# Kernel tuning notes

Hardware: AMD Instinct MI355X
Metric: run time of the kernel (lower is better)

## Reference

```python
import jax, jax.numpy as jnp
import numpy as np

NHEADS = 8
MIN_DEPTH = 0.5
MAX_DEPTH = 100.0


def _gather(img, xi, yi, nb, W, H):
    valid = (xi >= 0) & (xi < W) & (yi >= 0) & (yi < H)
    xc = jnp.clip(xi, 0, W - 1)
    yc = jnp.clip(yi, 0, H - 1)
    vals = img[nb, :, yc, xc]  # (N,Ho,Wo,C) - advanced idx dims come first
    return vals * valid[..., None].astype(img.dtype)


def grid_sample(img, grid, mode='bilinear'):
    # img: (N,C,H,W), grid: (N,Ho,Wo,2) in [-1,1], zeros padding, align_corners=True
    N, C, H, W = img.shape
    gx = (grid[..., 0] + 1.0) * 0.5 * (W - 1)
    gy = (grid[..., 1] + 1.0) * 0.5 * (H - 1)
    nb = jnp.arange(N)[:, None, None]
    if mode == 'nearest':
        out = _gather(img, jnp.round(gx).astype(jnp.int32), jnp.round(gy).astype(jnp.int32), nb, W, H)
    else:
        x0 = jnp.floor(gx); y0 = jnp.floor(gy)
        wx = (gx - x0)[..., None]; wy = (gy - y0)[..., None]
        x0i = x0.astype(jnp.int32); y0i = y0.astype(jnp.int32)
        g00 = _gather(img, x0i, y0i, nb, W, H)
        g01 = _gather(img, x0i + 1, y0i, nb, W, H)
        g10 = _gather(img, x0i, y0i + 1, nb, W, H)
        g11 = _gather(img, x0i + 1, y0i + 1, nb, W, H)
        out = (1 - wy) * ((1 - wx) * g00 + wx * g01) + wy * ((1 - wx) * g10 + wx * g11)
    return jnp.transpose(out, (0, 3, 1, 2))  # (N,C,Ho,Wo)


def _avg3(x):
    # 3x3 avg pool, stride 1, reflect pad 1 (output same HxW)
    xp = jnp.pad(x, ((0, 0), (0, 0), (1, 1), (1, 1)), mode='reflect')
    return jax.lax.reduce_window(xp, 0.0, jax.lax.add, (1, 1, 3, 3), (1, 1, 1, 1), 'VALID') / 9.0


def ssim_loss(x, y, C1=1e-4, C2=9e-4):
    mx, my = _avg3(x), _avg3(y)
    sx = _avg3(x * x) - mx * mx
    sy = _avg3(y * y) - my * my
    sxy = _avg3(x * y) - mx * my
    num = (2 * mx * my + C1) * (2 * sxy + C2)
    den = (mx * mx + my * my + C1) * (sx + sy + C2)
    return jnp.clip((1.0 - num / den) * 0.5, 0.0, 1.0)


def prepare_b(x):
    d, c, h, w = x.shape
    return x.transpose(0, 2, 3, 1).reshape(d, h * w, c)  # (seq=d, batch=h*w, c)


def layer_norm(x, g, b, eps=1e-5):
    m = x.mean(-1, keepdims=True)
    v = ((x - m) ** 2).mean(-1, keepdims=True)
    return (x - m) * jax.lax.rsqrt(v + eps) * g + b


def attention(q_in, kv_in, w_qkv, b_qkv, w_o, b_o):
    # q_in: (Lq,B,C), kv_in: (Lk,B,C)
    C = q_in.shape[-1]
    hd = C // NHEADS
    q = q_in @ w_qkv[:C].T + b_qkv[:C]
    kv = kv_in @ w_qkv[C:].T + b_qkv[C:]
    k, v = jnp.split(kv, 2, axis=-1)
    Lq, B = q.shape[0], q.shape[1]
    Lk = k.shape[0]
    q = (q * (hd ** -0.5)).reshape(Lq, B, NHEADS, hd)
    k = k.reshape(Lk, B, NHEADS, hd)
    v = v.reshape(Lk, B, NHEADS, hd)
    attn = jnp.einsum('wnhc,vnhc->nhwv', q, k)  # (B,H,Lq,Lk)
    p = jax.nn.softmax(attn, axis=-1)
    out = jnp.einsum('nhwv,vnhc->wnhc', p, v).reshape(Lq, B, C)
    out = out @ w_o.T + b_o
    raw = attn.sum(axis=1)  # (B,Lq,Lk)
    return out, raw


def _forward(feat1, feat2, coords, sa_in_w, sa_in_b, sa_out_w, sa_out_b, sa_ln_g, sa_ln_b,
             ca_in_w, ca_in_b, ca_out_w, ca_out_b, ca_ln_g, ca_ln_b, num_bins):
    bs, C, h, w = feat1.shape
    cg = jnp.where(coords < -1.0, -2.0, coords)
    cg = jnp.where(cg > 1.0, 2.0, cg)
    rep_feat2 = jnp.broadcast_to(feat2, (num_bins, C, h, w))
    warped = grid_sample(rep_feat2, cg, 'bilinear')  # (num_bins,C,h,w)
    ones = jnp.ones((num_bins, 1, h, w), feat1.dtype)
    warped_mask = grid_sample(ones, cg, 'nearest')
    # SSIM cost volume (no-grad side outputs)
    x = jnp.broadcast_to(feat1, warped.shape)
    ssim_volume = jax.lax.stop_gradient(ssim_loss(x, warped).mean(axis=1)[None])  # (1,num_bins,h,w)
    idx = jnp.argmin(ssim_volume, axis=1)  # (1,h,w)
    depth = jnp.exp(np.float32(np.log(MIN_DEPTH)) + np.float32(np.log(MAX_DEPTH / MIN_DEPTH)) * idx.astype(feat1.dtype) / (num_bins - 1))
    lowest_cost = 1.0 / depth
    f1 = prepare_b(feat1)   # (bs, h*w, C)
    f2 = prepare_b(warped)  # (num_bins, h*w, C)
    raw = None
    L = sa_in_w.shape[0]
    for i in range(L):
        f1n = layer_norm(f1, sa_ln_g[i], sa_ln_b[i])
        o, _ = attention(f1n, f1n, sa_in_w[i], sa_in_b[i], sa_out_w[i], sa_out_b[i])
        f1 = f1 + o
        f1n = layer_norm(f1, ca_ln_g[i], ca_ln_b[i])
        f2n = layer_norm(f2, ca_ln_g[i], ca_ln_b[i])
        o, raw = attention(f1n, f2n, ca_in_w[i], ca_in_b[i], ca_out_w[i], ca_out_b[i])
        f1 = f1 + o
    attn_weight = raw.reshape(bs, h, w, num_bins)
    return attn_weight, warped_mask, lowest_cost, ssim_volume


def setup_inputs():
    key = jax.random.key(0)
    ks = jax.random.split(key, 16)
    C, L, NB, H, W = 128, 6, 64, 48, 160
    s = 0.02
    return {
        'feat1': jax.random.normal(ks[0], (1, C, H, W), jnp.float32),
        'feat2': jax.random.normal(ks[1], (1, C, H, W), jnp.float32),
        'coords': jax.random.uniform(ks[2], (NB, H, W, 2), jnp.float32) * 2.4 - 1.2,
        'sa_in_w': jax.random.normal(ks[3], (L, 3 * C, C), jnp.float32) * s,
        'sa_in_b': jax.random.normal(ks[4], (L, 3 * C), jnp.float32) * s,
        'sa_out_w': jax.random.normal(ks[5], (L, C, C), jnp.float32) * s,
        'sa_out_b': jax.random.normal(ks[6], (L, C), jnp.float32) * s,
        'sa_ln_g': jnp.ones((L, C), jnp.float32),
        'sa_ln_b': jnp.zeros((L, C), jnp.float32),
        'ca_in_w': jax.random.normal(ks[7], (L, 3 * C, C), jnp.float32) * s,
        'ca_in_b': jax.random.normal(ks[8], (L, 3 * C), jnp.float32) * s,
        'ca_out_w': jax.random.normal(ks[9], (L, C, C), jnp.float32) * s,
        'ca_out_b': jax.random.normal(ks[10], (L, C), jnp.float32) * s,
        'ca_ln_g': jnp.ones((L, C), jnp.float32),
        'ca_ln_b': jnp.zeros((L, C), jnp.float32),
        'num_bins': NB,
    }


def reference(feat1, feat2, coords, sa_in_w, sa_in_b, sa_out_w, sa_out_b, sa_ln_g, sa_ln_b,
              ca_in_w, ca_in_b, ca_out_w, ca_out_b, ca_ln_g, ca_ln_b, num_bins):
    return _forward(feat1, feat2, coords, sa_in_w, sa_in_b, sa_out_w, sa_out_b, sa_ln_g, sa_ln_b,
                    ca_in_w, ca_in_b, ca_out_w, ca_out_b, ca_ln_g, ca_ln_b, num_bins)
```

## Files before the change

kernel.cpp:

```cpp
#include <hip/hip_runtime.h>

constexpr int kH  = 48;
constexpr int kW  = 160;
constexpr int kP  = 7680;
constexpr int kC  = 128;
constexpr int kNB = 64;
constexpr int kNH = 8;
constexpr int kNL = 6;

constexpr long long OFF_F1T = 0;
constexpr long long OFF_F2T = 983040;
constexpr long long OFF_F2  = 1966080;
constexpr long long OFF_MU  = OFF_F2 + 62914560LL;
constexpr long long OFF_SIG = OFF_MU + 491520LL;
constexpr long long OFF_WTS = OFF_SIG + 491520LL;
constexpr int WSA2 = 0;
constexpr int WQ2  = 8192;
constexpr int WKU  = 16384;
constexpr int WV2  = 24576;
constexpr int WO2  = 32768;
constexpr int BSA  = 40960;
constexpr int BQ   = 41088;
constexpr int BK   = 41216;
constexpr int BV   = 41344;
constexpr int WTS_STRIDE = 41472;

constexpr long long OUT_ATT  = 0;
constexpr long long OUT_MASK = 491520;
constexpr long long OUT_LC   = 983040;
constexpr long long OUT_SSIM = 990720;

typedef _Float16 h2v __attribute__((ext_vector_type(2)));
typedef __fp16 p2v __attribute__((ext_vector_type(2)));
typedef float f2v __attribute__((ext_vector_type(2)));
typedef __fp16 h8 __attribute__((ext_vector_type(8)));
typedef float fx16 __attribute__((ext_vector_type(16)));
union U32H2 { unsigned u; h2v h; };
union U32P2 { unsigned u; p2v h; };

__device__ __forceinline__ float fdot2(unsigned a, unsigned b, float c) {
  U32H2 ua; ua.u = a; U32H2 ub; ub.u = b;
  return __builtin_amdgcn_fdot2(ua.h, ub.h, c, false);
}
__device__ __forceinline__ unsigned pkrtz(float a, float b) {
  U32P2 t; t.h = __builtin_amdgcn_cvt_pkrtz(a, b); return t.u;
}
__device__ __forceinline__ f2v h2f(unsigned u) {
  U32P2 t; t.u = u; f2v r; r.x = (float)t.h.x; r.y = (float)t.h.y; return r;
}
__device__ __forceinline__ unsigned short f2h(float x) {
  U32P2 t; t.h = __builtin_amdgcn_cvt_pkrtz(x, 0.f); return (unsigned short)(t.u & 0xffffu);
}
__device__ __forceinline__ void wb() {
  __asm__ __volatile__("" ::: "memory");
  __builtin_amdgcn_wave_barrier();
  __asm__ __volatile__("" ::: "memory");
}

__global__ __launch_bounds__(256) void k_transpose(const float* __restrict__ feat1,
                                                   const float* __restrict__ feat2,
                                                   float* __restrict__ f1t,
                                                   float* __restrict__ f2t) {
  __shared__ float t1[32][33], t2[32][33];
  const int p0 = blockIdx.x * 32, c0 = blockIdx.y * 32;
  const int r = threadIdx.x >> 5, col = threadIdx.x & 31;
#pragma unroll
  for (int rr = r; rr < 32; rr += 8) {
    t1[rr][col] = feat1[(c0 + rr) * kP + p0 + col];
    t2[rr][col] = feat2[(c0 + rr) * kP + p0 + col];
  }
  __syncthreads();
#pragma unroll
  for (int rr = r; rr < 32; rr += 8) {
    f1t[(p0 + rr) * kC + c0 + col] = t1[col][rr];
    f2t[(p0 + rr) * kC + c0 + col] = t2[col][rr];
  }
}

__device__ __forceinline__ float redsum128(float v, float* red2) {
#pragma unroll
  for (int off = 32; off > 0; off >>= 1) v += __shfl_xor(v, off);
  int t = threadIdx.x;
  if ((t & 63) == 0) red2[t >> 6] = v;
  __syncthreads();
  float r = red2[0] + red2[1];
  __syncthreads();
  return r;
}

__global__ __launch_bounds__(128) void k_fold(
    const float* __restrict__ saw_, const float* __restrict__ sab_,
    const float* __restrict__ sow_, const float* __restrict__ sob_,
    const float* __restrict__ slg_, const float* __restrict__ slb_,
    const float* __restrict__ caw_, const float* __restrict__ cab_,
    const float* __restrict__ clg_, const float* __restrict__ clb_,
    const float* __restrict__ cow_, float* __restrict__ wts) {
  int i = blockIdx.x >> 7, d = blockIdx.x & 127, c = threadIdx.x;
  const float* saw = saw_ + (long long)i * 384 * kC;
  const float* sab = sab_ + i * 384;
  const float* sow = sow_ + i * kC * kC;
  const float* sob = sob_ + i * kC;
  const float* slg = slg_ + i * kC;
  const float* slb = slb_ + i * kC;
  const float* caw = caw_ + (long long)i * 384 * kC;
  const float* cab = cab_ + i * 384;
  const float* clg = clg_ + i * kC;
  const float* clb = clb_ + i * kC;
  const float* cow = cow_ + i * kC * kC;
  float* WL = wts + (long long)i * WTS_STRIDE;
  __shared__ float red2[2];

  int jstd = (c >> 3) * 1024 + d * 8 + (c & 7);

  float acc = 0.f;
  for (int m = 0; m < kC; m++) acc += sow[d * kC + m] * saw[(256 + m) * kC + c];
  float t1 = redsum128(acc * slb[c] + sow[d * kC + c] * sab[256 + c], red2);
  if (c == 0) WL[BSA + d] = t1 + sob[d];
  ((unsigned short*)(WL + WSA2))[jstd] = f2h(acc * slg[c]);

  float wq = caw[d * kC + c];
  float t2 = redsum128(wq * clb[c], red2);
  if (c == 0) WL[BQ + d] = 0.25f * (t2 + cab[d]);
  ((unsigned short*)(WL + WQ2))[jstd] = f2h(0.25f * wq * clg[c]);

  float wk = caw[(kC + d) * kC + c];
  float t3 = redsum128(wk * clb[c], red2);
  if (c == 0) WL[BK + d] = t3 + cab[kC + d];
  {
    int h = d >> 4, o = d & 15;
    ((unsigned short*)(WL + WKU))[h * 2048 + c * 16 + o] = f2h(wk * clg[c]);
  }

  float wv = caw[(2 * kC + d) * kC + c];
  float t4 = redsum128(wv * clb[c], red2);
  if (c == 0) WL[BV + d] = t4 + cab[2 * kC + d];
  ((unsigned short*)(WL + WV2))[jstd] = f2h(wv * clg[c]);

  ((unsigned short*)(WL + WO2))[jstd] = f2h(cow[d * kC + c]);
}

__global__ __launch_bounds__(256) void k_warp(const float* __restrict__ f2t,
                                              const float* __restrict__ coords,
                                              float* __restrict__ F2, float* __restrict__ mu,
                                              float* __restrict__ sig, float* __restrict__ maskout) {
  int wave = threadIdx.x >> 6, lane = threadIdx.x & 63;
  int pix = blockIdx.x * 4 + wave;
  int b = blockIdx.y;
  long long bp = (long long)b * kP + pix;
  float cx = coords[bp * 2], cy = coords[bp * 2 + 1];
  cx = (cx < -1.f) ? -2.f : cx;
  cx = (cx > 1.f) ? 2.f : cx;
  cy = (cy < -1.f) ? -2.f : cy;
  cy = (cy > 1.f) ? 2.f : cy;
  float gx = (cx + 1.f) * 0.5f * (float)(kW - 1);
  float gy = (cy + 1.f) * 0.5f * (float)(kH - 1);
  float x0f = floorf(gx), y0f = floorf(gy);
  float wx = gx - x0f, wy = gy - y0f;
  int x0 = (int)x0f, y0 = (int)y0f;
  int x1 = x0 + 1, y1 = y0 + 1;
  float vx0 = (x0 >= 0 && x0 < kW) ? 1.f : 0.f;
  float vx1 = (x1 >= 0 && x1 < kW) ? 1.f : 0.f;
  float vy0 = (y0 >= 0 && y0 < kH) ? 1.f : 0.f;
  float vy1 = (y1 >= 0 && y1 < kH) ? 1.f : 0.f;
  int x0c = min(max(x0, 0), kW - 1), x1c = min(max(x1, 0), kW - 1);
  int y0c = min(max(y0, 0), kH - 1), y1c = min(max(y1, 0), kH - 1);
  float w00 = (1.f - wy) * (1.f - wx) * vx0 * vy0;
  float w01 = (1.f - wy) * wx * vx1 * vy0;
  float w10 = wy * (1.f - wx) * vx0 * vy1;
  float w11 = wy * wx * vx1 * vy1;
  const float2* r00 = (const float2*)(f2t + (y0c * kW + x0c) * kC);
  const float2* r01 = (const float2*)(f2t + (y0c * kW + x1c) * kC);
  const float2* r10 = (const float2*)(f2t + (y1c * kW + x0c) * kC);
  const float2* r11 = (const float2*)(f2t + (y1c * kW + x1c) * kC);
  float2 g00 = r00[lane], g01 = r01[lane], g10 = r10[lane], g11 = r11[lane];
  float v0 = w00 * g00.x + w01 * g01.x + w10 * g10.x + w11 * g11.x;
  float v1 = w00 * g00.y + w01 * g01.y + w10 * g10.y + w11 * g11.y;
  float s = v0 + v1, s2 = v0 * v0 + v1 * v1;
#pragma unroll
  for (int off = 32; off > 0; off >>= 1) {
    s += __shfl_xor(s, off);
    s2 += __shfl_xor(s2, off);
  }
  float m = s * (1.f / 128.f);
  float var = s2 * (1.f / 128.f) - m * m;
  float rs = rsqrtf(var + 1e-5f);
  float2 o;
  o.x = (v0 - m) * rs;
  o.y = (v1 - m) * rs;
  ((float2*)(F2 + bp * kC))[lane] = o;
  if (lane == 0) {
    mu[bp] = m;
    sig[bp] = sqrtf(var + 1e-5f);
    int xi = (int)rintf(gx), yi = (int)rintf(gy);
    maskout[bp] = (xi >= 0 && xi < kW && yi >= 0 && yi < kH) ? 1.f : 0.f;
  }
}

__global__ __launch_bounds__(256) void k_ssim(const float* __restrict__ f1t,
                                              const float* __restrict__ F2,
                                              const float* __restrict__ mu,
                                              const float* __restrict__ sig,
                                              float* __restrict__ ssimout) {
  const int lane = threadIdx.x & 63;
  const int y = blockIdx.x * 4 + (threadIdx.x >> 6);
  const int b = blockIdx.y;
  const int ym = (y == 0) ? 1 : y - 1;
  const int yp = (y == kH - 1) ? kH - 2 : y + 1;
  const long long bb = (long long)b * kP;
  const float* f1m = f1t + (ym * kW) * kC + 2 * lane;
  const float* f10 = f1t + (y * kW) * kC + 2 * lane;
  const float* f1p = f1t + (yp * kW) * kC + 2 * lane;
  const float* F2m = F2 + (bb + ym * kW) * kC + 2 * lane;
  const float* F20 = F2 + (bb + y * kW) * kC + 2 * lane;
  const float* F2p = F2 + (bb + yp * kW) * kC + 2 * lane;
  const float* mum = mu + bb + ym * kW;
  const float* mu0 = mu + bb + y * kW;
  const float* mup = mu + bb + yp * kW;
  const float* sgm = sig + bb + ym * kW;
  const float* sg0 = sig + bb + y * kW;
  const float* sgp = sig + bb + yp * kW;
  float* outrow = ssimout + bb + y * kW;

  f2v C[3][5];

  auto colsum = [&](int x, f2v* Cc) {
    f2v am = *(const f2v*)(f1m + (size_t)x * kC);
    f2v a0 = *(const f2v*)(f10 + (size_t)x * kC);
    f2v ap = *(const f2v*)(f1p + (size_t)x * kC);
    f2v fm = *(const f2v*)(F2m + (size_t)x * kC);
    f2v f0 = *(const f2v*)(F20 + (size_t)x * kC);
    f2v fp = *(const f2v*)(F2p + (size_t)x * kC);
    f2v wm = fm * sgm[x] + mum[x];
    f2v w0 = f0 * sg0[x] + mu0[x];
    f2v wp = fp * sgp[x] + mup[x];
    Cc[0] = am + a0 + ap;
    Cc[1] = wm + w0 + wp;
    Cc[2] = am * am + a0 * a0 + ap * ap;
    Cc[3] = wm * wm + w0 * w0 + wp * wp;
    Cc[4] = am * wm + a0 * w0 + ap * wp;
  };

  auto emit = [&](int xo, f2v s0, f2v s1, f2v s2, f2v s3, f2v s4) {
    const float inv9 = 1.f / 9.f;
    f2v mx = s0 * inv9, my = s1 * inv9;
    f2v vx = s2 * inv9 - mx * mx;
    f2v vy = s3 * inv9 - my * my;
    f2v vxy = s4 * inv9 - mx * my;
    f2v num = (2.f * mx * my + 1e-4f) * (2.f * vxy + 9e-4f);
    f2v den = (mx * mx + my * my + 1e-4f) * (vx + vy + 9e-4f);
    f2v val = (1.f - num / den) * 0.5f;
    float t = fminf(fmaxf(val.x, 0.f), 1.f) + fminf(fmaxf(val.y, 0.f), 1.f);
#pragma unroll
    for (int o = 32; o > 0; o >>= 1) t += __shfl_xor(t, o);
    if (lane == 0) outrow[xo] = t * (1.f / 128.f);
  };

  colsum(0, C[0]);
  colsum(1, C[1]);
  emit(0, C[0][0] + 2.f * C[1][0], C[0][1] + 2.f * C[1][1], C[0][2] + 2.f * C[1][2],
       C[0][3] + 2.f * C[1][3], C[0][4] + 2.f * C[1][4]);
#pragma unroll 3
  for (int x = 2; x < kW; ++x) {
    colsum(x, C[x % 3]);
    emit(x - 1, C[0][0] + C[1][0] + C[2][0], C[0][1] + C[1][1] + C[2][1],
         C[0][2] + C[1][2] + C[2][2], C[0][3] + C[1][3] + C[2][3],
         C[0][4] + C[1][4] + C[2][4]);
  }
  emit(kW - 1, C[0][0] + 2.f * C[2][0], C[0][1] + 2.f * C[2][1], C[0][2] + 2.f * C[2][2],
       C[0][3] + 2.f * C[2][3], C[0][4] + 2.f * C[2][4]);
}

__global__ __launch_bounds__(256) void k_argmin(const float* __restrict__ ssim,
                                                float* __restrict__ lc) {
  int pix = blockIdx.x * 256 + threadIdx.x;
  float best = ssim[pix];
  int bi = 0;
  for (int b = 1; b < kNB; b++) {
    float v = ssim[b * kP + pix];
    if (v < best) { best = v; bi = b; }
  }
  float depth = expf(-0.69314718f + (5.2983174f * (float)bi) / 63.0f);
  lc[pix] = 1.f / depth;
}


__device__ __forceinline__ f2v gemmW(int l, const unsigned* __restrict__ inb,
                                     const unsigned* __restrict__ W, float b0, float b1) {
  float a0 = b0, a1 = b1, c0 = 0.f, c1 = 0.f;
  const unsigned* wp = W + l * 8;
#pragma unroll
  for (int j = 0; j < 16; j += 2) {
    uint4 inA = *(const uint4*)(inb + 4 * j);
    uint4 inB = *(const uint4*)(inb + 4 * j + 4);
    uint4 wa = *(const uint4*)(wp + j * 512);
    uint4 wc = *(const uint4*)(wp + j * 512 + 4);
    uint4 wa2 = *(const uint4*)(wp + j * 512 + 512);
    uint4 wc2 = *(const uint4*)(wp + j * 512 + 516);
    a0 = fdot2(inA.x, wa.x, a0);  a0 = fdot2(inA.y, wa.y, a0);
    a0 = fdot2(inA.z, wa.z, a0);  a0 = fdot2(inA.w, wa.w, a0);
    a1 = fdot2(inA.x, wc.x, a1);  a1 = fdot2(inA.y, wc.y, a1);
    a1 = fdot2(inA.z, wc.z, a1);  a1 = fdot2(inA.w, wc.w, a1);
    c0 = fdot2(inB.x, wa2.x, c0); c0 = fdot2(inB.y, wa2.y, c0);
    c0 = fdot2(inB.z, wa2.z, c0); c0 = fdot2(inB.w, wa2.w, c0);
    c1 = fdot2(inB.x, wc2.x, c1); c1 = fdot2(inB.y, wc2.y, c1);
    c1 = fdot2(inB.z, wc2.z, c1); c1 = fdot2(inB.w, wc2.w, c1);
  }
  f2v r; r.x = a0 + c0; r.y = a1 + c1; return r;
}

__device__ __forceinline__ void ln_store(int l, f2v X, unsigned* xhq) {
  float s = X.x + X.y, s2 = X.x * X.x + X.y * X.y;
#pragma unroll
  for (int o = 32; o > 0; o >>= 1) { s += __shfl_xor(s, o); s2 += __shfl_xor(s2, o); }
  float m = s * 0.0078125f;
  float var = s2 * 0.0078125f - m * m;
  float rs = rsqrtf(var + 1e-5f);
  xhq[l] = pkrtz((X.x - m) * rs, (X.y - m) * rs);
}

__global__ __launch_bounds__(64) void k_attn(const float* __restrict__ F2g,
                                             const float* __restrict__ f1t,
                                             const float* __restrict__ wts,
                                             const float* __restrict__ cab_out,
                                             float* __restrict__ attn_out) {
  __shared__ __align__(16) unsigned F2s[64 * 64];
  __shared__ __align__(16) unsigned upb[512];
  __shared__ __align__(16) unsigned xhq[64];

  const int l = threadIdx.x;
  const int pix = blockIdx.x;

  {
#pragma unroll 4
    for (int r = 0; r < 64; ++r) {
      float2 v = *(const float2*)(F2g + ((long long)r * kP + pix) * kC + 2 * l);
      F2s[r * 64 + (l ^ (4 * (r & 15)))] = pkrtz(v.x, v.y);
    }
  }
  f2v X;
  { float2 xv = ((const float2*)(f1t + (long long)pix * kC))[l]; X.x = xv.x; X.y = xv.y; }
  wb();

  float chsum = 0.f;
  float* pf = (float*)upb;
  const int mrow = l & 31;
  const int kg = l >> 5;
  const int rbase = 4 * kg;

  for (int ly = 0; ly < kNL; ++ly) {
    const float* WL = wts + (long long)ly * WTS_STRIDE;

    ln_store(l, X, xhq);
    wb();
    {
      float2 bv = ((const float2*)(WL + BSA))[l];
      f2v o = gemmW(l, xhq, (const unsigned*)(WL + WSA2), bv.x, bv.y);
      X += o;
    }
    wb();
    ln_store(l, X, xhq);
    wb();
    f2v q;
    {
      float2 bv = ((const float2*)(WL + BQ))[l];
      q = gemmW(l, xhq, (const unsigned*)(WL + WQ2), bv.x, bv.y);
    }
    if (ly == kNL - 1) {
      float2 bk = ((const float2*)(WL + BK))[l];
      float cp = q.x * bk.x + q.y * bk.y;
#pragma unroll
      for (int o = 32; o > 0; o >>= 1) cp += __shfl_xor(cp, o);
      chsum = cp;
    }
    xhq[l] = pkrtz(q.x, q.y);
    wb();

    {
      const unsigned* KU = (const unsigned*)(WL + WKU);
#pragma unroll
      for (int h = 0; h < kNH; ++h) {
        uint4 q0 = *(const uint4*)(xhq + h * 8);
        uint4 q1 = *(const uint4*)(xhq + h * 8 + 4);
        const unsigned* w0 = KU + (h * 128 + 2 * l) * 8;
        uint4 a0 = ((const uint4*)w0)[0], a1 = ((const uint4*)w0)[1];
        uint4 b0 = ((const uint4*)w0)[2], b1 = ((const uint4*)w0)[3];
        float u0 = 0.f, u1 = 0.f, u2 = 0.f, u3 = 0.f;
        u0 = fdot2(q0.x, a0.x, u0); u0 = fdot2(q0.y, a0.y, u0);
        u0 = fdot2(q0.z, a0.z, u0); u0 = fdot2(q0.w, a0.w, u0);
        u2 = fdot2(q1.x, a1.x, u2); u2 = fdot2(q1.y, a1.y, u2);
        u2 = fdot2(q1.z, a1.z, u2); u2 = fdot2(q1.w, a1.w, u2);
        u1 = fdot2(q0.x, b0.x, u1); u1 = fdot2(q0.y, b0.y, u1);
        u1 = fdot2(q0.z, b0.z, u1); u1 = fdot2(q0.w, b0.w, u1);
        u3 = fdot2(q1.x, b1.x, u3); u3 = fdot2(q1.y, b1.y, u3);
        u3 = fdot2(q1.z, b1.z, u3); u3 = fdot2(q1.w, b1.w, u3);
        upb[h * 64 + (l ^ (4 * h))] = pkrtz(u0 + u2, u1 + u3);
      }
    }
    wb();

    fx16 acc0 = (fx16)0.f, acc1 = (fx16)0.f;
    {
      const int hn = mrow & 7;
      const int sw = 4 * (mrow & 15);
      const int usw = 4 * hn;
#pragma unroll
      for (int kc = 0; kc < 8; ++kc) {
        const int cp = kc * 8 + kg * 4;
        h8 Bv = *(const h8*)(upb + hn * 64 + (cp ^ usw));
        h8 A0 = *(const h8*)(F2s + mrow * 64 + (cp ^ sw));
        h8 A1 = *(const h8*)(F2s + (mrow + 32) * 64 + (cp ^ sw));
        acc0 = __builtin_amdgcn_mfma_f32_32x32x16_f16(A0, Bv, acc0, 0, 0, 0);
        acc1 = __builtin_amdgcn_mfma_f32_32x32x16_f16(A1, Bv, acc1, 0, 0, 0);
      }
    }
    if (ly == kNL - 1) {
      wb();
      if (mrow < 8) {
#pragma unroll
        for (int r = 0; r < 16; ++r) {
          int row = (r & 3) + 8 * (r >> 2) + rbase;
          pf[mrow * 64 + row] = acc0[r];
          pf[mrow * 64 + 32 + row] = acc1[r];
        }
      }
      wb();
      float rsum = chsum;
#pragma unroll
      for (int h = 0; h < kNH; ++h) rsum += pf[h * 64 + l];
      attn_out[(long long)pix * 64 + l] = rsum;
      return;
    }
    {
      float mx = acc0[0];
#pragma unroll
      for (int r = 0; r < 16; ++r) { mx = fmaxf(mx, acc0[r]); mx = fmaxf(mx, acc1[r]); }
      mx = fmaxf(mx, __shfl_xor(mx, 32));
      float pv0[16], pv1[16];
      float sm = 0.f;
#pragma unroll
      for (int r = 0; r < 16; ++r) {
        pv0[r] = __expf(acc0[r] - mx); sm += pv0[r];
        pv1[r] = __expf(acc1[r] - mx); sm += pv1[r];
      }
      sm += __shfl_xor(sm, 32);
      float inv = 1.f / sm;
      wb();
      if (mrow < 8) {
#pragma unroll
        for (int r = 0; r < 16; ++r) {
          int row = (r & 3) + 8 * (r >> 2) + rbase;
          pf[row * 8 + mrow] = pv0[r] * inv;
          pf[(32 + row) * 8 + mrow] = pv1[r] * inv;
        }
      }
    }
    wb();
    {
      const int half = l >> 5, lb = l & 31;
      f2v wA[8], wB[8];
#pragma unroll
      for (int h = 0; h < kNH; ++h) { wA[h] = (f2v)0.f; wB[h] = (f2v)0.f; }
#pragma unroll 2
      for (int t = 0; t < 32; ++t) {
        int b = half * 32 + t;
        uint2 fv = *(const uint2*)(F2s + b * 64 + ((2 * lb) ^ (4 * (b & 15))));
        f2v fA = h2f(fv.x), fB = h2f(fv.y);
        float4 pA = *(const float4*)(pf + b * 8);
        float4 pB = *(const float4*)(pf + b * 8 + 4);
        wA[0] += fA * pA.x; wB[0] += fB * pA.x;
        wA[1] += fA * pA.y; wB[1] += fB * pA.y;
        wA[2] += fA * pA.z; wB[2] += fB * pA.z;
        wA[3] += fA * pA.w; wB[3] += fB * pA.w;
        wA[4] += fA * pB.x; wB[4] += fB * pB.x;
        wA[5] += fA * pB.y; wB[5] += fB * pB.y;
        wA[6] += fA * pB.z; wB[6] += fB * pB.z;
        wA[7] += fA * pB.w; wB[7] += fB * pB.w;
      }
#pragma unroll
      for (int h = 0; h < kNH; ++h) {
        wA[h].x += __shfl_xor(wA[h].x, 32);
        wA[h].y += __shfl_xor(wA[h].y, 32);
        wB[h].x += __shfl_xor(wB[h].x, 32);
        wB[h].y += __shfl_xor(wB[h].y, 32);
      }
      wb();
#pragma unroll
      for (int hh = 0; hh < 4; ++hh) {
        int h = half * 4 + hh;
        uint2 pk;
        pk.x = pkrtz(wA[h].x, wA[h].y);
        pk.y = pkrtz(wB[h].x, wB[h].y);
        *(uint2*)(upb + h * 64 + ((2 * lb) ^ (4 * h))) = pk;
      }
    }
    wb();
    {
      const int h = l >> 3;
      const unsigned* wrow = upb + h * 64;
      const unsigned* WV = (const unsigned*)(WL + WV2) + l * 8;
      float2 bv = ((const float2*)(WL + BV))[l];
      float a0 = bv.x, a1 = bv.y, c0 = 0.f, c1 = 0.f;
      const int sw = 4 * h;
#pragma unroll
      for (int j = 0; j < 16; j += 2) {
        uint4 inA = *(const uint4*)(wrow + ((4 * j) ^ sw));
        uint4 inB = *(const uint4*)(wrow + ((4 * j + 4) ^ sw));
        uint4 wa = *(const uint4*)(WV + j * 512);
        uint4 wc = *(const uint4*)(WV + j * 512 + 4);
        uint4 wa2 = *(const uint4*)(WV + j * 512 + 512);
        uint4 wc2 = *(const uint4*)(WV + j * 512 + 516);
        a0 = fdot2(inA.x, wa.x, a0);  a0 = fdot2(inA.y, wa.y, a0);
        a0 = fdot2(inA.z, wa.z, a0);  a0 = fdot2(inA.w, wa.w, a0);
        a1 = fdot2(inA.x, wc.x, a1);  a1 = fdot2(inA.y, wc.y, a1);
        a1 = fdot2(inA.z, wc.z, a1);  a1 = fdot2(inA.w, wc.w, a1);
        c0 = fdot2(inB.x, wa2.x, c0); c0 = fdot2(inB.y, wa2.y, c0);
        c0 = fdot2(inB.z, wa2.z, c0); c0 = fdot2(inB.w, wa2.w, c0);
        c1 = fdot2(inB.x, wc2.x, c1); c1 = fdot2(inB.y, wc2.y, c1);
        c1 = fdot2(inB.z, wc2.z, c1); c1 = fdot2(inB.w, wc2.w, c1);
      }
      xhq[l] = pkrtz(a0 + c0, a1 + c1);
    }
    wb();
    {
      float2 bv = ((const float2*)(cab_out + ly * kC))[l];
      f2v o = gemmW(l, xhq, (const unsigned*)(WL + WO2), bv.x, bv.y);
      X += o;
    }
    wb();
  }
}

extern "C" void kernel_launch(void* const* d_in, const int* in_sizes, int n_in, void* d_out,
                              int out_size, void* d_ws, size_t ws_size, hipStream_t stream) {
  (void)in_sizes; (void)n_in; (void)out_size; (void)ws_size;
  const float* feat1 = (const float*)d_in[0];
  const float* feat2 = (const float*)d_in[1];
  const float* coords = (const float*)d_in[2];
  const float* sa_in_w = (const float*)d_in[3];
  const float* sa_in_b = (const float*)d_in[4];
  const float* sa_out_w = (const float*)d_in[5];
  const float* sa_out_b = (const float*)d_in[6];
  const float* sa_ln_g = (const float*)d_in[7];
  const float* sa_ln_b = (const float*)d_in[8];
  const float* ca_in_w = (const float*)d_in[9];
  const float* ca_in_b = (const float*)d_in[10];
  const float* ca_out_w = (const float*)d_in[11];
  const float* ca_out_b = (const float*)d_in[12];
  const float* ca_ln_g = (const float*)d_in[13];
  const float* ca_ln_b = (const float*)d_in[14];

  float* out = (float*)d_out;
  float* ws = (float*)d_ws;
  float* f1t = ws + OFF_F1T;
  float* f2t = ws + OFF_F2T;
  float* F2 = ws + OFF_F2;
  float* mu = ws + OFF_MU;
  float* sig = ws + OFF_SIG;
  float* wts = ws + OFF_WTS;

  float* att = out + OUT_ATT;
  float* mask = out + OUT_MASK;
  float* lc = out + OUT_LC;
  float* ssim = out + OUT_SSIM;

  dim3 gt(240, 4);
  k_transpose<<<gt, 256, 0, stream>>>(feat1, feat2, f1t, f2t);
  k_fold<<<kNL * 128, 128, 0, stream>>>(sa_in_w, sa_in_b, sa_out_w, sa_out_b, sa_ln_g, sa_ln_b,
                                        ca_in_w, ca_in_b, ca_ln_g, ca_ln_b, ca_out_w, wts);
  dim3 g1(1920, 64);
  k_warp<<<g1, 256, 0, stream>>>(f2t, coords, F2, mu, sig, mask);
  dim3 g2(12, 64);
  k_ssim<<<g2, 256, 0, stream>>>(f1t, F2, mu, sig, ssim);
  k_argmin<<<30, 256, 0, stream>>>(ssim, lc);
  k_attn<<<kP, 64, 0, stream>>>(F2, f1t, wts, ca_out_b, att);
}
```

Baseline: 899.4 us.

## Stage layer weights into LDS with async double-buffering and reorder F2 pixel-major

The attention kernel now runs four pixels per 256-thread block. Per-layer fp16 weights are streamed in chunks into a double-buffered LDS region with global_load_lds, so the four waves share one copy instead of each reading weights from global memory. The warped feature tensor F2 is now written pixel-major so each pixel's 64 bins are contiguous. The attention kernel reads them directly from global and converts to fp16 on the fly, dropping the per-block LDS copy. The weight packing in the fold kernel is reordered to match the chunked LDS layout. The cost is block-wide __syncthreads between chunks and more global reads of F2 inside the layer loop, while k_ssim now reads F2 with a strided pattern.

```diff
diff --git a/kernel.cpp b/kernel.cpp
--- a/kernel.cpp
+++ b/kernel.cpp
@@ -7,6 +7,7 @@
 constexpr int kNB = 64;
 constexpr int kNH = 8;
 constexpr int kNL = 6;
+constexpr int kFS = kNB * kC;
 
 constexpr long long OFF_F1T = 0;
 constexpr long long OFF_F2T = 983040;
@@ -45,9 +46,6 @@
 __device__ __forceinline__ unsigned pkrtz(float a, float b) {
   U32P2 t; t.h = __builtin_amdgcn_cvt_pkrtz(a, b); return t.u;
 }
-__device__ __forceinline__ f2v h2f(unsigned u) {
-  U32P2 t; t.u = u; f2v r; r.x = (float)t.h.x; r.y = (float)t.h.y; return r;
-}
 __device__ __forceinline__ unsigned short f2h(float x) {
   U32P2 t; t.h = __builtin_amdgcn_cvt_pkrtz(x, 0.f); return (unsigned short)(t.u & 0xffffu);
 }
@@ -55,6 +53,19 @@
   __asm__ __volatile__("" ::: "memory");
   __builtin_amdgcn_wave_barrier();
   __asm__ __volatile__("" ::: "memory");
+}
+
+typedef __attribute__((address_space(1))) const void gvoid_t;
+typedef __attribute__((address_space(3))) void svoid_t;
+__device__ __forceinline__ void gl_lds16(const unsigned* g, unsigned* s) {
+  __builtin_amdgcn_global_load_lds((gvoid_t*)g, (svoid_t*)s, 16, 0, 0);
+}
+__device__ __forceinline__ void stage_chunk(const unsigned* W32, int c, unsigned* buf,
+                                            int w, int l) {
+  const unsigned* s = W32 + c * 2048 + w * 512 + l * 4;
+  unsigned* d = buf + w * 512;
+  gl_lds16(s, d);
+  gl_lds16(s + 256, d + 256);
 }
 
 __global__ __launch_bounds__(256) void k_transpose(const float* __restrict__ feat1,
@@ -110,7 +121,7 @@
   float* WL = wts + (long long)i * WTS_STRIDE;
   __shared__ float red2[2];
 
-  int jstd = (c >> 3) * 1024 + d * 8 + (c & 7);
+  int jstd = (c >> 3) * 1024 + (d & 1) * 512 + (d >> 1) * 8 + (c & 7);
 
   float acc = 0.f;
   for (int m = 0; m < kC; m++) acc += sow[d * kC + m] * saw[(256 + m) * kC + c];
@@ -127,8 +138,10 @@
   float t3 = redsum128(wk * clb[c], red2);
   if (c == 0) WL[BK + d] = t3 + cab[kC + d];
   {
-    int h = d >> 4, o = d & 15;
-    ((unsigned short*)(WL + WKU))[h * 2048 + c * 16 + o] = f2h(wk * clg[c]);
+    int h = d >> 4, o = d & 15, op = o >> 1;
+    int q = (c & 1) * 2 + (op >> 2);
+    ((unsigned short*)(WL + WKU))[h * 2048 + q * 512 + (c >> 1) * 8 + (op & 3) * 2 + (o & 1)] =
+        f2h(wk * clg[c]);
   }
 
   float wv = caw[(2 * kC + d) * kC + c];
@@ -141,7 +154,8 @@
 
 __global__ __launch_bounds__(256) void k_warp(const float* __restrict__ f2t,
                                               const float* __restrict__ coords,
-                                              float* __restrict__ F2, float* __restrict__ mu,
+                                              float* __restrict__ F2,
+                                              float* __restrict__ mu,
                                               float* __restrict__ sig, float* __restrict__ maskout) {
   int wave = threadIdx.x >> 6, lane = threadIdx.x & 63;
   int pix = blockIdx.x * 4 + wave;
@@ -187,7 +201,7 @@
   float2 o;
   o.x = (v0 - m) * rs;
   o.y = (v1 - m) * rs;
-  ((float2*)(F2 + bp * kC))[lane] = o;
+  ((float2*)(F2 + ((long long)pix * kNB + b) * kC))[lane] = o;
   if (lane == 0) {
     mu[bp] = m;
     sig[bp] = sqrtf(var + 1e-5f);
@@ -210,9 +224,9 @@
   const float* f1m = f1t + (ym * kW) * kC + 2 * lane;
   const float* f10 = f1t + (y * kW) * kC + 2 * lane;
   const float* f1p = f1t + (yp * kW) * kC + 2 * lane;
-  const float* F2m = F2 + (bb + ym * kW) * kC + 2 * lane;
-  const float* F20 = F2 + (bb + y * kW) * kC + 2 * lane;
-  const float* F2p = F2 + (bb + yp * kW) * kC + 2 * lane;
+  const float* F2m = F2 + ((long long)(ym * kW) * kNB + b) * kC + 2 * lane;
+  const float* F20 = F2 + ((long long)(y * kW) * kNB + b) * kC + 2 * lane;
+  const float* F2p_ = F2 + ((long long)(yp * kW) * kNB + b) * kC + 2 * lane;
   const float* mum = mu + bb + ym * kW;
   const float* mu0 = mu + bb + y * kW;
   const float* mup = mu + bb + yp * kW;
@@ -227,9 +241,9 @@
     f2v am = *(const f2v*)(f1m + (size_t)x * kC);
     f2v a0 = *(const f2v*)(f10 + (size_t)x * kC);
     f2v ap = *(const f2v*)(f1p + (size_t)x * kC);
-    f2v fm = *(const f2v*)(F2m + (size_t)x * kC);
-    f2v f0 = *(const f2v*)(F20 + (size_t)x * kC);
-    f2v fp = *(const f2v*)(F2p + (size_t)x * kC);
+    f2v fm = *(const f2v*)(F2m + (size_t)x * kFS);
+    f2v f0 = *(const f2v*)(F20 + (size_t)x * kFS);
+    f2v fp = *(const f2v*)(F2p_ + (size_t)x * kFS);
     f2v wm = fm * sgm[x] + mum[x];
     f2v w0 = f0 * sg0[x] + mu0[x];
     f2v wp = fp * sgp[x] + mup[x];
@@ -284,29 +298,7 @@
 }
 
 
-__device__ __forceinline__ f2v gemmW(int l, const unsigned* __restrict__ inb,
-                                     const unsigned* __restrict__ W, float b0, float b1) {
-  float a0 = b0, a1 = b1, c0 = 0.f, c1 = 0.f;
-  const unsigned* wp = W + l * 8;
-#pragma unroll
-  for (int j = 0; j < 16; j += 2) {
-    uint4 inA = *(const uint4*)(inb + 4 * j);
-    uint4 inB = *(const uint4*)(inb + 4 * j + 4);
-    uint4 wa = *(const uint4*)(wp + j * 512);
-    uint4 wc = *(const uint4*)(wp + j * 512 + 4);
-    uint4 wa2 = *(const uint4*)(wp + j * 512 + 512);
-    uint4 wc2 = *(const uint4*)(wp + j * 512 + 516);
-    a0 = fdot2(inA.x, wa.x, a0);  a0 = fdot2(inA.y, wa.y, a0);
-    a0 = fdot2(inA.z, wa.z, a0);  a0 = fdot2(inA.w, wa.w, a0);
-    a1 = fdot2(inA.x, wc.x, a1);  a1 = fdot2(inA.y, wc.y, a1);
-    a1 = fdot2(inA.z, wc.z, a1);  a1 = fdot2(inA.w, wc.w, a1);
-    c0 = fdot2(inB.x, wa2.x, c0); c0 = fdot2(inB.y, wa2.y, c0);
-    c0 = fdot2(inB.z, wa2.z, c0); c0 = fdot2(inB.w, wa2.w, c0);
-    c1 = fdot2(inB.x, wc2.x, c1); c1 = fdot2(inB.y, wc2.y, c1);
-    c1 = fdot2(inB.z, wc2.z, c1); c1 = fdot2(inB.w, wc2.w, c1);
-  }
-  f2v r; r.x = a0 + c0; r.y = a1 + c1; return r;
-}
+constexpr int NW = 4;
 
 __device__ __forceinline__ void ln_store(int l, f2v X, unsigned* xhq) {
   float s = X.x + X.y, s2 = X.x * X.x + X.y * X.y;
@@ -318,54 +310,94 @@
   xhq[l] = pkrtz((X.x - m) * rs, (X.y - m) * rs);
 }
 
-__global__ __launch_bounds__(64) void k_attn(const float* __restrict__ F2g,
-                                             const float* __restrict__ f1t,
-                                             const float* __restrict__ wts,
-                                             const float* __restrict__ cab_out,
-                                             float* __restrict__ attn_out) {
-  __shared__ __align__(16) unsigned F2s[64 * 64];
-  __shared__ __align__(16) unsigned upb[512];
-  __shared__ __align__(16) unsigned xhq[64];
-
-  const int l = threadIdx.x;
-  const int pix = blockIdx.x;
-
-  {
-#pragma unroll 4
-    for (int r = 0; r < 64; ++r) {
-      float2 v = *(const float2*)(F2g + ((long long)r * kP + pix) * kC + 2 * l);
-      F2s[r * 64 + (l ^ (4 * (r & 15)))] = pkrtz(v.x, v.y);
-    }
-  }
-  f2v X;
-  { float2 xv = ((const float2*)(f1t + (long long)pix * kC))[l]; X.x = xv.x; X.y = xv.y; }
-  wb();
-
-  float chsum = 0.f;
+__device__ __forceinline__ void dot16(uint4 inA, uint4 inB, uint4 wa, uint4 wc,
+                                      uint4 wa2, uint4 wc2,
+                                      float& a0, float& a1, float& c0, float& c1) {
+  a0 = fdot2(inA.x, wa.x, a0);  a0 = fdot2(inA.y, wa.y, a0);
+  a0 = fdot2(inA.z, wa.z, a0);  a0 = fdot2(inA.w, wa.w, a0);
+  a1 = fdot2(inA.x, wc.x, a1);  a1 = fdot2(inA.y, wc.y, a1);
+  a1 = fdot2(inA.z, wc.z, a1);  a1 = fdot2(inA.w, wc.w, a1);
+  c0 = fdot2(inB.x, wa2.x, c0); c0 = fdot2(inB.y, wa2.y, c0);
+  c0 = fdot2(inB.z, wa2.z, c0); c0 = fdot2(inB.w, wa2.w, c0);
+  c1 = fdot2(inB.x, wc2.x, c1); c1 = fdot2(inB.y, wc2.y, c1);
+  c1 = fdot2(inB.z, wc2.z, c1); c1 = fdot2(inB.w, wc2.w, c1);
+}
+
+__device__ __forceinline__ void gemm_chunk(const unsigned* inb, const unsigned* wbp, int l,
+                                           float& a0, float& a1, float& c0, float& c1) {
+#pragma unroll
+  for (int jj = 0; jj < 4; jj += 2) {
+    uint4 inA = *(const uint4*)(inb + 4 * jj);
+    uint4 inB = *(const uint4*)(inb + 4 * jj + 4);
+    const unsigned* w0 = wbp + jj * 512 + l * 4;
+    uint4 wa = *(const uint4*)(w0);
+    uint4 wc = *(const uint4*)(w0 + 256);
+    uint4 wa2 = *(const uint4*)(w0 + 512);
+    uint4 wc2 = *(const uint4*)(w0 + 768);
+    dot16(inA, inB, wa, wc, wa2, wc2, a0, a1, c0, c1);
+  }
+}
+
+__global__ __launch_bounds__(256, 4) void k_attn(const float* __restrict__ F2f,
+                                                 const float* __restrict__ f1t,
+                                                 const float* __restrict__ wts,
+                                                 const float* __restrict__ cab_out,
+                                                 float* __restrict__ attn_out) {
+  __shared__ __align__(16) unsigned shw[NW * 576];
+  __shared__ __align__(16) unsigned wbuf[2][2048];
+
+  const int tid = threadIdx.x;
+  const int w = tid >> 6, l = tid & 63;
+  const int pix = blockIdx.x * NW + w;
+  unsigned* upb = shw + w * 576;
+  unsigned* xhq = upb + 512;
   float* pf = (float*)upb;
+  const float* F2p = F2f + (long long)pix * kFS;
+
   const int mrow = l & 31;
   const int kg = l >> 5;
   const int rbase = 4 * kg;
 
+  f2v X;
+  { float2 xv = ((const float2*)(f1t + (long long)pix * kC))[l]; X.x = xv.x; X.y = xv.y; }
+
+  stage_chunk((const unsigned*)wts, 0, wbuf[0], w, l);
+  __syncthreads();
+
+  float chsum = 0.f;
   for (int ly = 0; ly < kNL; ++ly) {
     const float* WL = wts + (long long)ly * WTS_STRIDE;
+    const unsigned* W32 = (const unsigned*)WL;
+    const bool last = (ly == kNL - 1);
 
     ln_store(l, X, xhq);
     wb();
     {
       float2 bv = ((const float2*)(WL + BSA))[l];
-      f2v o = gemmW(l, xhq, (const unsigned*)(WL + WSA2), bv.x, bv.y);
-      X += o;
-    }
-    wb();
+      float a0 = bv.x, a1 = bv.y, c0 = 0.f, c1 = 0.f;
+#pragma unroll
+      for (int c = 0; c < 4; ++c) {
+        stage_chunk(W32, c + 1, wbuf[(c + 1) & 1], w, l);
+        gemm_chunk(xhq + 16 * c, wbuf[c & 1], l, a0, a1, c0, c1);
+        __syncthreads();
+      }
+      X.x += a0 + c0; X.y += a1 + c1;
+    }
     ln_store(l, X, xhq);
     wb();
     f2v q;
     {
       float2 bv = ((const float2*)(WL + BQ))[l];
-      q = gemmW(l, xhq, (const unsigned*)(WL + WQ2), bv.x, bv.y);
-    }
-    if (ly == kNL - 1) {
+      float a0 = bv.x, a1 = bv.y, c0 = 0.f, c1 = 0.f;
+#pragma unroll
+      for (int c = 4; c < 8; ++c) {
+        stage_chunk(W32, c + 1, wbuf[(c + 1) & 1], w, l);
+        gemm_chunk(xhq + 16 * (c - 4), wbuf[c & 1], l, a0, a1, c0, c1);
+        __syncthreads();
+      }
+      q.x = a0 + c0; q.y = a1 + c1;
+    }
+    if (last) {
       float2 bk = ((const float2*)(WL + BK))[l];
       float cp = q.x * bk.x + q.y * bk.y;
 #pragma unroll
@@ -375,45 +407,58 @@
     xhq[l] = pkrtz(q.x, q.y);
     wb();
 
-    {
-      const unsigned* KU = (const unsigned*)(WL + WKU);
-#pragma unroll
-      for (int h = 0; h < kNH; ++h) {
+#pragma unroll
+    for (int c = 8; c < 12; ++c) {
+      if (!(last && c == 11)) stage_chunk(W32, c + 1, wbuf[(c + 1) & 1], w, l);
+      const unsigned* wbp = wbuf[c & 1];
+#pragma unroll
+      for (int hh = 0; hh < 2; ++hh) {
+        const int h = (c - 8) * 2 + hh;
         uint4 q0 = *(const uint4*)(xhq + h * 8);
         uint4 q1 = *(const uint4*)(xhq + h * 8 + 4);
-        const unsigned* w0 = KU + (h * 128 + 2 * l) * 8;
-        uint4 a0 = ((const uint4*)w0)[0], a1 = ((const uint4*)w0)[1];
-        uint4 b0 = ((const uint4*)w0)[2], b1 = ((const uint4*)w0)[3];
+        const unsigned* w0 = wbp + hh * 1024 + l * 4;
+        uint4 av0 = *(const uint4*)(w0);
+        uint4 av1 = *(const uint4*)(w0 + 256);
+        uint4 bv0 = *(const uint4*)(w0 + 512);
+        uint4 bv1 = *(const uint4*)(w0 + 768);
         float u0 = 0.f, u1 = 0.f, u2 = 0.f, u3 = 0.f;
-        u0 = fdot2(q0.x, a0.x, u0); u0 = fdot2(q0.y, a0.y, u0);
-        u0 = fdot2(q0.z, a0.z, u0); u0 = fdot2(q0.w, a0.w, u0);
-        u2 = fdot2(q1.x, a1.x, u2); u2 = fdot2(q1.y, a1.y, u2);
-        u2 = fdot2(q1.z, a1.z, u2); u2 = fdot2(q1.w, a1.w, u2);
-        u1 = fdot2(q0.x, b0.x, u1); u1 = fdot2(q0.y, b0.y, u1);
-        u1 = fdot2(q0.z, b0.z, u1); u1 = fdot2(q0.w, b0.w, u1);
-        u3 = fdot2(q1.x, b1.x, u3); u3 = fdot2(q1.y, b1.y, u3);
-        u3 = fdot2(q1.z, b1.z, u3); u3 = fdot2(q1.w, b1.w, u3);
+        u0 = fdot2(q0.x, av0.x, u0); u0 = fdot2(q0.y, av0.y, u0);
+        u0 = fdot2(q0.z, av0.z, u0); u0 = fdot2(q0.w, av0.w, u0);
+        u2 = fdot2(q1.x, av1.x, u2); u2 = fdot2(q1.y, av1.y, u2);
+        u2 = fdot2(q1.z, av1.z, u2); u2 = fdot2(q1.w, av1.w, u2);
+        u1 = fdot2(q0.x, bv0.x, u1); u1 = fdot2(q0.y, bv0.y, u1);
+        u1 = fdot2(q0.z, bv0.z, u1); u1 = fdot2(q0.w, bv0.w, u1);
+        u3 = fdot2(q1.x, bv1.x, u3); u3 = fdot2(q1.y, bv1.y, u3);
+        u3 = fdot2(q1.z, bv1.z, u3); u3 = fdot2(q1.w, bv1.w, u3);
         upb[h * 64 + (l ^ (4 * h))] = pkrtz(u0 + u2, u1 + u3);
       }
-    }
-    wb();
+      __syncthreads();
+    }
 
     fx16 acc0 = (fx16)0.f, acc1 = (fx16)0.f;
     {
       const int hn = mrow & 7;
-      const int sw = 4 * (mrow & 15);
       const int usw = 4 * hn;
+      const float* pA0 = F2p + mrow * kC + kg * 8;
+      const float* pA1 = F2p + (mrow + 32) * kC + kg * 8;
 #pragma unroll
       for (int kc = 0; kc < 8; ++kc) {
         const int cp = kc * 8 + kg * 4;
         h8 Bv = *(const h8*)(upb + hn * 64 + (cp ^ usw));
-        h8 A0 = *(const h8*)(F2s + mrow * 64 + (cp ^ sw));
-        h8 A1 = *(const h8*)(F2s + (mrow + 32) * 64 + (cp ^ sw));
-        acc0 = __builtin_amdgcn_mfma_f32_32x32x16_f16(A0, Bv, acc0, 0, 0, 0);
-        acc1 = __builtin_amdgcn_mfma_f32_32x32x16_f16(A1, Bv, acc1, 0, 0, 0);
-      }
-    }
-    if (ly == kNL - 1) {
+        float4 fa = *(const float4*)(pA0 + kc * 16);
+        float4 fb = *(const float4*)(pA0 + kc * 16 + 4);
+        float4 fc = *(const float4*)(pA1 + kc * 16);
+        float4 fd = *(const float4*)(pA1 + kc * 16 + 4);
+        union { unsigned u[4]; h8 h; } A0u, A1u;
+        A0u.u[0] = pkrtz(fa.x, fa.y); A0u.u[1] = pkrtz(fa.z, fa.w);
+        A0u.u[2] = pkrtz(fb.x, fb.y); A0u.u[3] = pkrtz(fb.z, fb.w);
+        A1u.u[0] = pkrtz(fc.x, fc.y); A1u.u[1] = pkrtz(fc.z, fc.w);
+        A1u.u[2] = pkrtz(fd.x, fd.y); A1u.u[3] = pkrtz(fd.z, fd.w);
+        acc0 = __builtin_amdgcn_mfma_f32_32x32x16_f16(A0u.h, Bv, acc0, 0, 0, 0);
+        acc1 = __builtin_amdgcn_mfma_f32_32x32x16_f16(A1u.h, Bv, acc1, 0, 0, 0);
+      }
+    }
+    if (last) {
       wb();
       if (mrow < 8) {
 #pragma unroll
@@ -457,14 +502,16 @@
     wb();
     {
       const int half = l >> 5, lb = l & 31;
+      const float* F2c = F2p + 4 * lb;
       f2v wA[8], wB[8];
 #pragma unroll
       for (int h = 0; h < kNH; ++h) { wA[h] = (f2v)0.f; wB[h] = (f2v)0.f; }
 #pragma unroll 2
       for (int t = 0; t < 32; ++t) {
         int b = half * 32 + t;
-        uint2 fv = *(const uint2*)(F2s + b * 64 + ((2 * lb) ^ (4 * (b & 15))));
-        f2v fA = h2f(fv.x), fB = h2f(fv.y);
+        float4 fv = *(const float4*)(F2c + b * kC);
+        f2v fA, fB;
+        fA.x = fv.x; fA.y = fv.y; fB.x = fv.z; fB.y = fv.w;
         float4 pA = *(const float4*)(pf + b * 8);
         float4 pB = *(const float4*)(pf + b * 8 + 4);
         wA[0] += fA * pA.x; wB[0] += fB * pA.x;
@@ -495,38 +542,42 @@
     }
     wb();
     {
-      const int h = l >> 3;
+      const int h = l >> 3, sw = 4 * h;
       const unsigned* wrow = upb + h * 64;
-      const unsigned* WV = (const unsigned*)(WL + WV2) + l * 8;
       float2 bv = ((const float2*)(WL + BV))[l];
       float a0 = bv.x, a1 = bv.y, c0 = 0.f, c1 = 0.f;
-      const int sw = 4 * h;
-#pragma unroll
-      for (int j = 0; j < 16; j += 2) {
-        uint4 inA = *(const uint4*)(wrow + ((4 * j) ^ sw));
-        uint4 inB = *(const uint4*)(wrow + ((4 * j + 4) ^ sw));
-        uint4 wa = *(const uint4*)(WV + j * 512);
-        uint4 wc = *(const uint4*)(WV + j * 512 + 4);
-        uint4 wa2 = *(const uint4*)(WV + j * 512 + 512);
-        uint4 wc2 = *(const uint4*)(WV + j * 512 + 516);
-        a0 = fdot2(inA.x, wa.x, a0);  a0 = fdot2(inA.y, wa.y, a0);
-        a0 = fdot2(inA.z, wa.z, a0);  a0 = fdot2(inA.w, wa.w, a0);
-        a1 = fdot2(inA.x, wc.x, a1);  a1 = fdot2(inA.y, wc.y, a1);
-        a1 = fdot2(inA.z, wc.z, a1);  a1 = fdot2(inA.w, wc.w, a1);
-        c0 = fdot2(inB.x, wa2.x, c0); c0 = fdot2(inB.y, wa2.y, c0);
-        c0 = fdot2(inB.z, wa2.z, c0); c0 = fdot2(inB.w, wa2.w, c0);
-        c1 = fdot2(inB.x, wc2.x, c1); c1 = fdot2(inB.y, wc2.y, c1);
-        c1 = fdot2(inB.z, wc2.z, c1); c1 = fdot2(inB.w, wc2.w, c1);
+#pragma unroll
+      for (int c = 12; c < 16; ++c) {
+        stage_chunk(W32, c + 1, wbuf[(c + 1) & 1], w, l);
+#pragma unroll
+        for (int jj = 0; jj < 4; jj += 2) {
+          const int j = (c - 12) * 4 + jj;
+          uint4 inA = *(const uint4*)(wrow + ((4 * j) ^ sw));
+          uint4 inB = *(const uint4*)(wrow + ((4 * j + 4) ^ sw));
+          const unsigned* w0 = wbuf[c & 1] + jj * 512 + l * 4;
+          uint4 wa = *(const uint4*)(w0);
+          uint4 wc = *(const uint4*)(w0 + 256);
+          uint4 wa2 = *(const uint4*)(w0 + 512);
+          uint4 wc2 = *(const uint4*)(w0 + 768);
+          dot16(inA, inB, wa, wc, wa2, wc2, a0, a1, c0, c1);
+        }
+        __syncthreads();
       }
       xhq[l] = pkrtz(a0 + c0, a1 + c1);
     }
     wb();
     {
       float2 bv = ((const float2*)(cab_out + ly * kC))[l];
-      f2v o = gemmW(l, xhq, (const unsigned*)(WL + WO2), bv.x, bv.y);
-      X += o;
-    }
-    wb();
+      float a0 = bv.x, a1 = bv.y, c0 = 0.f, c1 = 0.f;
+#pragma unroll
+      for (int c = 16; c < 20; ++c) {
+        const unsigned* Wn = (c == 19) ? (const unsigned*)(WL + WTS_STRIDE) : W32;
+        stage_chunk(Wn, (c == 19) ? 0 : c + 1, wbuf[(c + 1) & 1], w, l);
+        gemm_chunk(xhq + 16 * (c - 16), wbuf[c & 1], l, a0, a1, c0, c1);
+        __syncthreads();
+      }
+      X.x += a0 + c0; X.y += a1 + c1;
+    }
   }
 }
 
@@ -572,5 +623,5 @@
   dim3 g2(12, 64);
   k_ssim<<<g2, 256, 0, stream>>>(f1t, F2, mu, sig, ssim);
   k_argmin<<<30, 256, 0, stream>>>(ssim, lc);
-  k_attn<<<kP, 64, 0, stream>>>(F2, f1t, wts, ca_out_b, att);
-}
+  k_attn<<<kP / NW, 64 * NW, 0, stream>>>(F2, f1t, wts, ca_out_b, att);
+}
```

Result: slower. 964.4 us (+7.2%).
